# Kernel optimization log

Measured on AMD Instinct MI355X. Metric: run time of the kernel, lower is better.

The kernel has to match this reference:

```python
import jax, jax.numpy as jnp
import numpy as np


def conv1x1(x, W, b=None):
    # 1x1 conv == channel matmul: x (B,C,H,W), W (O,C)
    y = jnp.einsum('oc,bchw->bohw', W, x)
    if b is not None:
        y = y + b[None, :, None, None]
    return y


def setup_inputs() -> dict:
    key = jax.random.key(0)
    ks = jax.random.split(key, 20)
    B, C_l, C_h, H, W, d = 2, 64, 192, 64, 64, 128
    s = 0.02
    return {
        'll': jax.random.normal(ks[0], (B, C_l, H, W), jnp.float32),
        'hf': jax.random.normal(ks[1], (B, C_h, H, W), jnp.float32),
        'Wqh': jax.random.normal(ks[2], (d, C_h), jnp.float32) * s,
        'Wkh': jax.random.normal(ks[3], (d, C_h), jnp.float32) * s,
        'Wvh': jax.random.normal(ks[4], (d, C_h), jnp.float32) * s,
        'Wql': jax.random.normal(ks[5], (d, C_l), jnp.float32) * s,
        'Wkl': jax.random.normal(ks[6], (d, C_l), jnp.float32) * s,
        'Wvl': jax.random.normal(ks[7], (d, C_l), jnp.float32) * s,
        'Wph': jax.random.normal(ks[8], (C_h, d), jnp.float32) * s,
        'bph': jnp.zeros((C_h,), jnp.float32),
        'Wpl': jax.random.normal(ks[9], (C_l, d), jnp.float32) * s,
        'bpl': jnp.zeros((C_l,), jnp.float32),
        'Wah': jax.random.normal(ks[10], (C_h, C_h), jnp.float32) * s,
        'bah': jnp.zeros((C_h,), jnp.float32),
        'Wal': jax.random.normal(ks[11], (C_l, C_l), jnp.float32) * s,
        'bal': jnp.zeros((C_l,), jnp.float32),
        'alpha': jnp.ones((4,), jnp.float32),
    }


def reference(ll, hf, Wqh, Wkh, Wvh, Wql, Wkl, Wvl, Wph, bph, Wpl, bpl,
              Wah, bah, Wal, bal, alpha):
    B, C_l, H, W = ll.shape
    d = Wqh.shape[0]
    N = H * W
    scl = d ** (-0.5)

    Qh = conv1x1(hf, Wqh).reshape(B, d, N)
    Kh = conv1x1(hf, Wkh).reshape(B, d, N)
    Vh = conv1x1(hf, Wvh).reshape(B, d, N)
    Ql = conv1x1(ll, Wql).reshape(B, d, N)
    Kl = conv1x1(ll, Wkl).reshape(B, d, N)
    Vl = conv1x1(ll, Wvl).reshape(B, d, N)

    wdir = jax.nn.softmax(alpha)  # [row, col, diag, global]

    def sdpa(q, k, v):  # q,k,v: (B, L, d)
        a = jax.nn.softmax(jnp.einsum('bqd,bkd->bqk', q, k) * scl, axis=-1)
        return jnp.einsum('bqk,bkd->bqd', a, v)

    # ---- global: full N x N cross attention ----
    OL = sdpa(Qh.transpose(0, 2, 1), Kl.transpose(0, 2, 1), Vl.transpose(0, 2, 1)).transpose(0, 2, 1)
    OH = sdpa(Ql.transpose(0, 2, 1), Kh.transpose(0, 2, 1), Vh.transpose(0, 2, 1)).transpose(0, 2, 1)
    out_ll = conv1x1(OL.reshape(B, d, H, W), Wpl, bpl) * wdir[3]
    out_hf = conv1x1(OH.reshape(B, d, H, W), Wph, bph) * wdir[3]

    # ---- axial (row / col) attention ----
    def axial(q, k, v, row):
        perm = (0, 2, 3, 1) if row else (0, 3, 2, 1)  # (B,S,L,d)
        qr = q.reshape(B, d, H, W).transpose(perm)
        kr = k.reshape(B, d, H, W).transpose(perm)
        vr = v.reshape(B, d, H, W).transpose(perm)
        a = jax.nn.softmax(jnp.einsum('bsqd,bskd->bsqk', qr, kr) * scl, axis=-1)
        o = jnp.einsum('bsqk,bskd->bsqd', a, vr)
        inv = (0, 3, 1, 2) if row else (0, 3, 2, 1)
        return o.transpose(inv)  # (B,d,H,W)

    out_ll = out_ll + conv1x1(axial(Qh, Kl, Vl, True), Wpl, bpl) * wdir[0]
    out_hf = out_hf + conv1x1(axial(Ql, Kh, Vh, True), Wph, bph) * wdir[0]
    out_ll = out_ll + conv1x1(axial(Qh, Kl, Vl, False), Wpl, bpl) * wdir[1]
    out_hf = out_hf + conv1x1(axial(Ql, Kh, Vh, False), Wph, bph) * wdir[1]

    # ---- diag: faithful to original code (gather by diag index, attend, scatter back) ----
    i = jnp.arange(H)[:, None]
    j = jnp.arange(W)[None, :]
    flat_idx = (j - i + (H - 1)).reshape(-1)  # (N,), values in [0, H+W-2]

    def dsel(x):  # (B,d,N) -> (B,N,d) gathered along position axis
        return x[:, :, flat_idx].transpose(0, 2, 1)

    Ld = sdpa(dsel(Qh), dsel(Kl), dsel(Vl)).transpose(0, 2, 1)  # (B,d,N)
    Hd = sdpa(dsel(Ql), dsel(Kh), dsel(Vh)).transpose(0, 2, 1)
    blank_l = jnp.zeros((B, d, N), Ld.dtype).at[:, :, flat_idx].set(Ld)
    blank_h = jnp.zeros((B, d, N), Hd.dtype).at[:, :, flat_idx].set(Hd)
    out_ll = out_ll + conv1x1(blank_l.reshape(B, d, H, W), Wpl, bpl) * wdir[2]
    out_hf = out_hf + conv1x1(blank_h.reshape(B, d, H, W), Wph, bph) * wdir[2]

    ll_out = conv1x1(ll + out_ll, Wal, bal)
    hf_out = conv1x1(hf + out_hf, Wah, bah)
    return (ll_out, hf_out)
```

## Files before the change

kernel.cpp:

```cpp
#include <hip/hip_runtime.h>
#include <math.h>

#define N_  4096
#define D_  128
#define B_  2
#define CL_ 64
#define CH_ 192

typedef __attribute__((ext_vector_type(8))) short short8;
typedef __attribute__((ext_vector_type(4))) float f32x4;
typedef __attribute__((ext_vector_type(16))) float f32x16;

#if __has_builtin(__builtin_amdgcn_exp2f)
#define EXP2(x) __builtin_amdgcn_exp2f(x)
#else
#define EXP2(x) exp2f(x)
#endif

__device__ __forceinline__ short f2bf(float x) {
  union { float f; unsigned u; } v; v.f = x;
  unsigned r = v.u + 0x7FFFu + ((v.u >> 16) & 1u);
  return (short)(r >> 16);
}

typedef __attribute__((address_space(1))) const void gv_t;
typedef __attribute__((address_space(3))) void sv_t;
__device__ __forceinline__ void gl_lds16(const void* g, void* l) {
  __builtin_amdgcn_global_load_lds((gv_t*)g, (sv_t*)l, 16, 0, 0);
}

#define CVTPK(d, lo, hi) asm("v_cvt_pk_bf16_f32 %0, %1, %2" : "=v"(d) : "v"(lo), "v"(hi))
#define PLSWAP(a, b) asm("v_permlane32_swap_b32 %0, %1" : "+v"(a), "+v"(b))

__global__ __launch_bounds__(256)
void vt_kernel(const short* __restrict__ Vhb, const short* __restrict__ Vlb,
               short* __restrict__ Vht, short* __restrict__ Vlt) {
  __shared__ short rowbuf[4 * 4096];
  const int tid = threadIdx.x;
  const int lane = tid & 63, w = tid >> 6;
  const short* src = blockIdx.y ? Vlb : Vhb;
  short* dst = blockIdx.y ? Vlt : Vht;
  const int r0 = blockIdx.x * 4;
  #pragma unroll
  for (int i = 0; i < 8; ++i) {
    int idx = i * 256 + w * 64 + lane;
    int row = idx >> 9, g = idx & 511;
    gl_lds16(src + (size_t)(r0 + row) * N_ + g * 8,
             (char*)rowbuf + i * 4096 + w * 1024 + lane * 16);
  }
  __syncthreads();
  const int rw = r0 + w, d7 = rw & 7;
  const short* rb = rowbuf + w * 4096;
  const int w0 = (lane & 7) * 8, h0 = (lane >> 3) * 8;
  short8 rr[8];
  #pragma unroll
  for (int j = 0; j < 8; ++j)
    rr[j] = *(const short8*)(rb + (h0 + j) * 64 + (((w0 >> 3) ^ d7) * 8));
  #pragma unroll
  for (int i = 0; i < 8; ++i) {
    short8 o;
    #pragma unroll
    for (int j = 0; j < 8; ++j) o[j] = rr[j][i];
    *(short8*)(dst + (size_t)rw * N_ + (w0 + i) * 64 + (((h0 >> 3) ^ d7) * 8)) = o;
  }
}

struct QkvP {
  const float *W0h, *W1h, *W2h, *W0l, *W1l, *W2l;
  const float *Xh, *Xl;
  short *QbH, *KbH, *VbH, *QtH, *KtH;
  short *QbL, *KbL, *VbL, *QtL, *KtL;
  float qscale;
};

__global__ __launch_bounds__(256, 3)
void qkv_kernel(QkvP g) {
  __shared__ __align__(16) char BT[24576];
  __shared__ __align__(16) char AS[8192];
  __shared__ __align__(16) float Ls[64][67];
  const int tid = threadIdx.x;
  const int lane = tid & 63, w = tid >> 6, m = lane & 15, hi = lane >> 4;
  const int n0 = blockIdx.x * 64;
  const int sel = blockIdx.y >> 1, dhalf = blockIdx.y & 1, ot0 = dhalf * 64;
  const int b = blockIdx.z >> 1, s = blockIdx.z & 1;
  const int C = s ? CL_ : CH_;
  const float* Wm = s ? (sel == 0 ? g.W0l : sel == 1 ? g.W1l : g.W2l)
                      : (sel == 0 ? g.W0h : sel == 1 ? g.W1h : g.W2h);
  const float* Xs = (s ? g.Xl : g.Xh) + (size_t)b * C * N_;
  const int C2 = C * 2;

  for (int cc = 0; cc < C; cc += 64) {
    #pragma unroll
    for (int r = 0; r < 16; ++r) {
      int flat = r * 256 + tid;
      int c = flat >> 6, nn = flat & 63;
      Ls[c][nn] = Xs[(size_t)(cc + c) * N_ + n0 + nn];
    }
    __syncthreads();
    #pragma unroll
    for (int e = 0; e < 2; ++e) {
      int u = e * 256 + tid;
      int nn = u >> 3, gl = u & 7;
      short8 v;
      #pragma unroll
      for (int j = 0; j < 8; ++j) v[j] = f2bf(Ls[gl*8 + j][nn]);
      int pos = (gl ^ (nn & 7)) & 7;
      *(short8*)(BT + nn * C2 + cc * 2 + pos * 16) = v;
    }
    __syncthreads();
  }

  f32x4 acc[4];
  #pragma unroll
  for (int i = 0; i < 4; ++i) acc[i] = (f32x4){0.f, 0.f, 0.f, 0.f};

  for (int c0 = 0; c0 < C; c0 += 64) {
    __syncthreads();
    {
      int o = tid >> 2, cq = tid & 3;
      const float* wp = Wm + (size_t)(ot0 + o) * C + c0 + cq * 16;
      float4 fa = *(const float4*)(wp + 0);
      float4 fb = *(const float4*)(wp + 4);
      float4 fc = *(const float4*)(wp + 8);
      float4 fd = *(const float4*)(wp + 12);
      short8 v0 = { f2bf(fa.x), f2bf(fa.y), f2bf(fa.z), f2bf(fa.w),
                    f2bf(fb.x), f2bf(fb.y), f2bf(fb.z), f2bf(fb.w) };
      short8 v1 = { f2bf(fc.x), f2bf(fc.y), f2bf(fc.z), f2bf(fc.w),
                    f2bf(fd.x), f2bf(fd.y), f2bf(fd.z), f2bf(fd.w) };
      int g0 = cq * 2;
      *(short8*)(AS + o * 128 + (((g0) ^ (o & 7)) * 16)) = v0;
      *(short8*)(AS + o * 128 + (((g0 + 1) ^ (o & 7)) * 16)) = v1;
    }
    __syncthreads();
    const int orow = w * 16 + m;
    short8 a0 = *(const short8*)(AS + orow * 128 + (((hi) ^ (orow & 7)) * 16));
    short8 a1 = *(const short8*)(AS + orow * 128 + (((4 + hi) ^ (orow & 7)) * 16));
    #pragma unroll
    for (int nf = 0; nf < 4; ++nf) {
      int nrow = nf * 16 + m;
      const char* brow = BT + nrow * C2 + c0 * 2;
      short8 b0 = *(const short8*)(brow + (((hi) ^ (nrow & 7)) * 16));
      short8 b1 = *(const short8*)(brow + (((4 + hi) ^ (nrow & 7)) * 16));
      acc[nf] = __builtin_amdgcn_mfma_f32_16x16x32_bf16(a0, b0, acc[nf], 0, 0, 0);
      acc[nf] = __builtin_amdgcn_mfma_f32_16x16x32_bf16(a1, b1, acc[nf], 0, 0, 0);
    }
  }

  __syncthreads();
  #pragma unroll
  for (int nf = 0; nf < 4; ++nf)
    #pragma unroll
    for (int r = 0; r < 4; ++r)
      Ls[w * 16 + hi * 4 + r][nf * 16 + m] = acc[nf][r];
  __syncthreads();

  if (sel < 2) {
    float sc = (sel == 0) ? g.qscale : 1.f;
    short* QK = (sel == 0 ? (s ? g.QbL : g.QbH) : (s ? g.KbL : g.KbH)) + (size_t)b * N_ * D_;
    short* QKt = (sel == 0 ? (s ? g.QtL : g.QtH) : (s ? g.KtL : g.KtH)) + (size_t)b * N_ * D_;
    const int bx = blockIdx.x;
    #pragma unroll
    for (int e = 0; e < 2; ++e) {
      int u = tid + 256 * e;
      int nn = u >> 3, gl = u & 7;
      short8 v;
      #pragma unroll
      for (int j = 0; j < 8; ++j) v[j] = f2bf(Ls[gl*8 + j][nn] * sc);
      int posb = (dhalf * 8) | ((gl ^ (nn & 7)) & 7);
      *(short8*)(QK + (size_t)(n0 + nn) * D_ + posb * 8) = v;
      int post = (dhalf * 8) | ((gl ^ (bx & 7)) & 7);
      *(short8*)(QKt + (size_t)(nn * 64 + bx) * D_ + post * 8) = v;
    }
  } else {
    short* Vb = (s ? g.VbL : g.VbH) + (size_t)b * D_ * N_;
    #pragma unroll
    for (int e = 0; e < 2; ++e) {
      int u = tid + 256 * e;
      int o = u >> 3, gl = u & 7;
      int d = ot0 + o;
      short8 v;
      #pragma unroll
      for (int j = 0; j < 8; ++j) v[j] = f2bf(Ls[o][gl*8 + j]);
      *(short8*)(Vb + (size_t)d * N_ + n0 + ((gl ^ (d & 7)) * 8)) = v;
    }
  }
}

struct SmP {
  const short *Qhb, *Qlb, *Khb, *Klb, *Vhb, *Vlb;
  const short *Qht, *Qlt, *Kht, *Klt, *Vht, *Vlt;
  float *Mrl, *Mrh, *Mcl, *Mch, *Mdl, *Mdh;
  const float* alpha;
};

__global__ __launch_bounds__(256, 3)
void attn_sm(SmP p) {
  __shared__ __align__(16) char smem[49152];
  const int tid = threadIdx.x;
  const int lane = tid & 63, w = tid >> 6, m = lane & 15, hi = lane >> 4;

  const int bxg = blockIdx.x;
  int variant, y, bz, qx;
  if (bxg < 256)      { variant = 0; y = bxg & 63;        bz = bxg >> 6;        qx = 0; }
  else if (bxg < 512) { variant = 1; y = (bxg-256) & 63;  bz = (bxg-256) >> 6;  qx = 0; }
  else                { variant = 2; y = 0;               bz = (bxg-512) >> 1;  qx = (bxg-512) & 1; }
  const int b = bz >> 1, pair = bz & 1;
  const int widx = variant;
  const int cwflag = (variant == 2);
  const int qbase = (variant == 2) ? qx * 64 : y * 64;
  const int kcol0 = (variant == 2) ? 0 : y * 64;
  const int Lk = (variant == 2) ? 127 : 64;
  const int lqloc = (variant == 2) ? (qx ? 63 : 64) : 64;

  const short *Qs, *Ks, *Vs;
  if (variant == 1) {
    Qs = pair ? p.Qlt : p.Qht; Ks = pair ? p.Kht : p.Klt; Vs = pair ? p.Vht : p.Vlt;
  } else {
    Qs = pair ? p.Qlb : p.Qhb; Ks = pair ? p.Khb : p.Klb; Vs = pair ? p.Vhb : p.Vlb;
  }
  Qs += (size_t)b * N_ * D_; Ks += (size_t)b * N_ * D_; Vs += (size_t)b * D_ * N_;
  float* Mout;
  if (variant == 0)      Mout = (pair ? p.Mrh : p.Mrl) + (size_t)b * D_ * N_;
  else if (variant == 1) Mout = (pair ? p.Mch : p.Mcl) + (size_t)b * D_ * N_;
  else                   Mout = (pair ? p.Mdh : p.Mdl) + (size_t)b * D_ * 128;

  float a0 = p.alpha[0], a1 = p.alpha[1], a2 = p.alpha[2], a3 = p.alpha[3];
  float am = fmaxf(fmaxf(a0, a1), fmaxf(a2, a3));
  float e0 = __expf(a0-am), e1 = __expf(a1-am), e2 = __expf(a2-am), e3 = __expf(a3-am);
  float wsel = (widx == 0 ? e0 : widx == 1 ? e1 : e2) / (e0 + e1 + e2 + e3);

  auto stageK = [&](int kt) {
    #pragma unroll
    for (int i = 0; i < 4; ++i) {
      int chunk = w * 4 + i;
      gl_lds16(Ks + (size_t)(kcol0 + kt*64) * D_ + chunk * 512 + lane * 8,
               smem + 16384 + chunk * 1024);
    }
  };
  auto stageV = [&](int kt) {
    #pragma unroll
    for (int i = 0; i < 4; ++i) {
      int chunk = w * 4 + i;
      gl_lds16(Vs + (size_t)(chunk*8 + (lane>>3)) * N_ + kcol0 + kt*64 + (lane&7)*8,
               smem + 32768 + chunk * 1024);
    }
  };
  #pragma unroll
  for (int i = 0; i < 4; ++i) {
    int chunk = w * 4 + i;
    gl_lds16(Qs + (size_t)qbase * D_ + chunk * 512 + lane * 8, smem + chunk * 1024);
  }
  stageK(0); stageV(0);
  __syncthreads();

  const int qrow = w * 16 + m;
  short8 qf[4];
  #pragma unroll
  for (int cs = 0; cs < 4; ++cs)
    qf[cs] = *(const short8*)(smem + qrow * 256 + ((cs*64 + hi*16) ^ ((qrow & 7) << 4)));
  __syncthreads();

  f32x4 oacc[8];
  #pragma unroll
  for (int i = 0; i < 8; ++i) oacc[i] = (f32x4){0.f, 0.f, 0.f, 0.f};
  float m_run[4] = {-INFINITY, -INFINITY, -INFINITY, -INFINITY};
  float l_run[4] = {0.f, 0.f, 0.f, 0.f};
  char* const pstrip = smem + w * 2048;
  const int NT = (Lk + 63) >> 6;

  for (int kt = 0; kt < NT; ++kt) {
    const char* Kc = smem + 16384;
    const char* Vc = smem + 32768;
    f32x4 sacc[4];
    #pragma unroll
    for (int kf = 0; kf < 4; ++kf) sacc[kf] = (f32x4){0.f, 0.f, 0.f, 0.f};
    #pragma unroll
    for (int kf = 0; kf < 4; ++kf) {
      const int krow = kf * 16 + m;
      const char* kr = Kc + krow * 256;
      #pragma unroll
      for (int cs = 0; cs < 4; ++cs) {
        short8 kfr = *(const short8*)(kr + ((cs*64 + hi*16) ^ ((krow & 7) << 4)));
        sacc[kf] = __builtin_amdgcn_mfma_f32_16x16x32_bf16(qf[cs], kfr, sacc[kf], 0, 0, 0);
      }
    }
    float cw[4];
    #pragma unroll
    for (int kf = 0; kf < 4; ++kf) {
      if (cwflag) {
        int kg = kt * 64 + kf * 16 + m;
        int dd = kg - 63; dd = dd < 0 ? -dd : dd;
        cw[kf] = (kg < Lk) ? (float)(64 - dd) : 0.f;
      } else cw[kf] = 1.f;
    }
    #pragma unroll
    for (int r = 0; r < 4; ++r) {
      float mt = fmaxf(fmaxf(sacc[0][r], sacc[1][r]), fmaxf(sacc[2][r], sacc[3][r]));
      mt = fmaxf(mt, __shfl_xor(mt, 1));
      mt = fmaxf(mt, __shfl_xor(mt, 2));
      mt = fmaxf(mt, __shfl_xor(mt, 4));
      mt = fmaxf(mt, __shfl_xor(mt, 8));
      float mn = fmaxf(m_run[r], mt);
      float corr = EXP2(m_run[r] - mn);
      m_run[r] = mn;
      const int rl = hi * 4 + r;
      char* prow = pstrip + rl * 128;
      float psum = 0.f;
      #pragma unroll
      for (int kf = 0; kf < 4; ++kf) {
        float pv = cw[kf] * EXP2(sacc[kf][r] - mn);
        psum += pv;
        int kcol = (kf * 16 + m) * 2;
        *(short*)(prow + (kcol ^ ((rl & 7) << 4))) = f2bf(pv);
      }
      psum += __shfl_xor(psum, 1);
      psum += __shfl_xor(psum, 2);
      psum += __shfl_xor(psum, 4);
      psum += __shfl_xor(psum, 8);
      l_run[r] = l_run[r] * corr + psum;
      #pragma unroll
      for (int cf = 0; cf < 8; ++cf) oacc[cf][r] *= corr;
    }
    #pragma unroll
    for (int ks = 0; ks < 2; ++ks) {
      short8 pa = *(const short8*)(pstrip + m * 128 + ((ks*64 + hi*16) ^ ((m & 7) << 4)));
      #pragma unroll
      for (int cf = 0; cf < 8; ++cf) {
        const int crow = cf * 16 + m;
        short8 vf = *(const short8*)(Vc + crow * 128 + ((ks*64 + hi*16) ^ ((crow & 7) << 4)));
        oacc[cf] = __builtin_amdgcn_mfma_f32_16x16x32_bf16(pa, vf, oacc[cf], 0, 0, 0);
      }
    }
    __syncthreads();
    if (kt + 1 < NT) { stageK(kt + 1); stageV(kt + 1); __syncthreads(); }
  }

  float inv[4];
  #pragma unroll
  for (int r = 0; r < 4; ++r) inv[r] = wsel / l_run[r];
  float* Os = (float*)smem;
  #pragma unroll
  for (int cf = 0; cf < 8; ++cf)
    #pragma unroll
    for (int r = 0; r < 4; ++r)
      Os[(cf*16 + m) * 66 + w * 16 + hi * 4 + r] = oacc[cf][r] * inv[r];
  __syncthreads();
  for (int it = 0; it < 32; ++it) {
    int flat = it * 256 + tid;
    int c = flat >> 6, qq = flat & 63;
    if (qq < lqloc) {
      float v = Os[c * 66 + qq];
      if (variant == 0)      Mout[(size_t)c * N_ + qbase + qq] = v;
      else if (variant == 1) Mout[(size_t)c * N_ + qq * 64 + y] = v;
      else                   Mout[c * 128 + qbase + qq] = v;
    }
  }
}

#define GVQ 65536

struct GlobalAttnParams {
  const short *Qhb, *Qlb, *Khb, *Klb, *Vhb, *Vlb;
  const float *Mrl, *Mrh, *Mcl, *Mch, *Mdl, *Mdh;
  short *Mtbl, *Mtbh;
  const float* alpha;
};

__global__ __launch_bounds__(512, 1)
void attn_gl_kernel(GlobalAttnParams p) {
  __shared__ __align__(16) char smem[131072];
  const int tid = threadIdx.x;
  const int lane = tid & 63, w = tid >> 6;
  const int wid = w & 1, gsel = w >> 1;
  const int key = lane & 31, kh = lane >> 5;

  const int bx = blockIdx.x;
  const int xcd = bx & 7, sub = bx >> 3;
  const int pz = xcd >> 1;
  const int b = pz >> 1, pair = pz & 1;
  const int q0 = ((xcd & 1) * 32 + sub) * 64;

  const short* Qb = (pair ? p.Qlb : p.Qhb) + (size_t)b * N_ * D_;
  const short* Kb = (pair ? p.Khb : p.Klb) + (size_t)b * N_ * D_;
  const short* Vb = (pair ? p.Vhb : p.Vlb) + (size_t)b * D_ * N_;
  const float* Mr = (pair ? p.Mrh : p.Mrl) + (size_t)b * D_ * N_;
  const float* Mc = (pair ? p.Mch : p.Mcl) + (size_t)b * D_ * N_;
  const float* Md = (pair ? p.Mdh : p.Mdl) + (size_t)b * D_ * 128;
  short* Mtb = (pair ? p.Mtbh : p.Mtbl) + (size_t)b * N_ * D_;

  float a0 = p.alpha[0], a1 = p.alpha[1], a2 = p.alpha[2], a3 = p.alpha[3];
  float am = fmaxf(fmaxf(a0,a1), fmaxf(a2,a3));
  float e0 = __expf(a0-am), e1 = __expf(a1-am), e2 = __expf(a2-am), e3 = __expf(a3-am);
  const float wsel = e3 / (e0+e1+e2+e3);

  auto stageQuad = [&](int qd) {
    #pragma unroll
    for (int i = 0; i < 8; ++i) {
      int c = w*8 + i;
      if (c < 32) {
        int tk = c >> 3, ck = c & 7;
        gl_lds16(Kb + (size_t)((4*qd + tk)*32 + ck*4)*D_ + lane*8,
                 smem + (qd & 1)*32768 + tk*8192 + ck*1024);
      } else {
        int cc = c - 32;
        int d = cc*4 + (lane >> 4);
        int g = lane & 15, kb2 = g >> 3, gg = g & 7;
        gl_lds16(Vb + (size_t)d*N_ + qd*128 + kb2*64 + ((gg ^ (d & 7))*8),
                 smem + GVQ + (qd & 1)*32768 + cc*1024);
      }
    }
  };

  const int qq = wid*32 + key;
  const short* qrow_g = Qb + (size_t)(q0 + qq) * D_;
  short8 qf[8];
  #pragma unroll
  for (int fi = 0; fi < 8; ++fi)
    qf[fi] = *(const short8*)(qrow_g + (((fi*2 + kh) ^ (qq & 7)) << 3));

  stageQuad(0);

  f32x16 oacc[4];
  #pragma unroll
  for (int d = 0; d < 4; ++d)
    #pragma unroll
    for (int r = 0; r < 16; ++r) oacc[d][r] = 0.f;
  float m_run = -INFINITY, l_run = 0.f;

  const int NQ = N_ / 128;
  for (int j = 0; j < NQ; ++j) {
    __syncthreads();
    if (j + 1 < NQ) stageQuad(j + 1);

    const char* Kc = smem + (j & 1)*32768 + gsel*8192;
    const char* Vc = smem + GVQ + (j & 1)*32768;

    f32x16 sacc;
    #pragma unroll
    for (int r = 0; r < 16; ++r) sacc[r] = 0.f;
    __builtin_amdgcn_s_setprio(1);
    #pragma unroll
    for (int fi = 0; fi < 8; ++fi) {
      short8 kf = *(const short8*)(Kc + key*256 + (((fi*2 + kh) ^ (key & 7)) << 4));
      sacc = __builtin_amdgcn_mfma_f32_32x32x16_bf16(kf, qf[fi], sacc, 0, 0, 0);
    }
    __builtin_amdgcn_s_setprio(0);

    float mt = sacc[0];
    #pragma unroll
    for (int r = 1; r < 16; ++r) mt = fmaxf(mt, sacc[r]);
    { float aa = mt, bb = mt; PLSWAP(aa, bb); mt = fmaxf(aa, bb); }
    if (!__all(mt <= m_run + 8.f)) {
      float mn = fmaxf(m_run, mt);
      float corr = EXP2(m_run - mn);
      m_run = mn;
      l_run *= corr;
      #pragma unroll
      for (int d = 0; d < 4; ++d)
        #pragma unroll
        for (int r = 0; r < 16; ++r) oacc[d][r] *= corr;
    }
    float pv[16];
    float psum = 0.f;
    #pragma unroll
    for (int r = 0; r < 16; ++r) { pv[r] = EXP2(sacc[r] - m_run); psum += pv[r]; }
    { float sa = psum, sb = psum; PLSWAP(sa, sb); psum = sa + sb; }
    l_run += psum;

    union U8 { unsigned u[4]; short8 s; } pf0, pf1;
    {
      unsigned c0, c1, c2, c3;
      CVTPK(c0, pv[0], pv[1]);  CVTPK(c1, pv[2], pv[3]);
      CVTPK(c2, pv[4], pv[5]);  CVTPK(c3, pv[6], pv[7]);
      PLSWAP(c0, c2); PLSWAP(c1, c3);
      pf0.u[0] = c0; pf0.u[1] = c1; pf0.u[2] = c2; pf0.u[3] = c3;
      CVTPK(c0, pv[8],  pv[9]);  CVTPK(c1, pv[10], pv[11]);
      CVTPK(c2, pv[12], pv[13]); CVTPK(c3, pv[14], pv[15]);
      PLSWAP(c0, c2); PLSWAP(c1, c3);
      pf1.u[0] = c0; pf1.u[1] = c1; pf1.u[2] = c2; pf1.u[3] = c3;
    }

    __builtin_amdgcn_s_setprio(1);
    #pragma unroll
    for (int d = 0; d < 4; ++d) {
      #pragma unroll
      for (int ks = 0; ks < 2; ++ks) {
        int crow = d*32 + key;
        int gidx = gsel*4 + ks*2 + kh;
        int kb2 = gidx >> 3, gg = gidx & 7;
        short8 vf = *(const short8*)(Vc + crow*256 + kb2*128 + ((gg ^ (key & 7)) << 4));
        oacc[d] = __builtin_amdgcn_mfma_f32_32x32x16_bf16(vf, (ks ? pf1.s : pf0.s), oacc[d], 0, 0, 0);
      }
    }
    __builtin_amdgcn_s_setprio(0);
  }
  __syncthreads();

  float* MLbase = (float*)(smem + 98304);
  if (gsel > 0) {
    int idx = (gsel - 1)*2 + wid;
    float* ob = (float*)smem + idx*4096;
    #pragma unroll
    for (int d = 0; d < 4; ++d)
      #pragma unroll
      for (int r = 0; r < 16; ++r)
        ob[(d*16 + r)*64 + lane] = oacc[d][r];
    float* ml = MLbase + idx*128;
    ml[lane] = m_run;
    ml[64 + lane] = l_run;
  }
  __syncthreads();

  float inv = 0.f;
  if (gsel == 0) {
    float mp[3], lp[3];
    float mn = m_run;
    #pragma unroll
    for (int pi = 0; pi < 3; ++pi) {
      const float* ml = MLbase + (pi*2 + wid)*128;
      mp[pi] = ml[lane]; lp[pi] = ml[64 + lane];
      mn = fmaxf(mn, mp[pi]);
    }
    float cA = EXP2(m_run - mn);
    float lt = l_run * cA;
    #pragma unroll
    for (int d = 0; d < 4; ++d)
      #pragma unroll
      for (int r = 0; r < 16; ++r) oacc[d][r] *= cA;
    #pragma unroll
    for (int pi = 0; pi < 3; ++pi) {
      float cp = EXP2(mp[pi] - mn);
      lt += lp[pi] * cp;
      const float* ob = (const float*)smem + (pi*2 + wid)*4096;
      #pragma unroll
      for (int d = 0; d < 4; ++d)
        #pragma unroll
        for (int r = 0; r < 16; ++r)
          oacc[d][r] += ob[(d*16 + r)*64 + lane] * cp;
    }
    inv = wsel / lt;
  }
  __syncthreads();

  float* Os = (float*)smem;
  if (gsel == 0) {
    #pragma unroll
    for (int d = 0; d < 4; ++d)
      #pragma unroll
      for (int r = 0; r < 16; ++r) {
        int dr = d*32 + (r & 3) + 8*(r >> 2) + 4*kh;
        Os[dr*66 + qq] = oacc[d][r] * inv;
      }
  }
  __syncthreads();

  for (int it = 0; it < 16; ++it) {
    int flat = it*512 + tid;
    int c = flat >> 6, q2 = flat & 63;
    int pos = q0 + q2;
    float add = Mr[(size_t)c*N_ + pos] + Mc[(size_t)c*N_ + pos];
    if (pos < 127) add += Md[c*128 + pos];
    Os[c*66 + q2] += add;
  }
  __syncthreads();
  #pragma unroll
  for (int e = 0; e < 2; ++e) {
    int u = tid + 512*e;
    int nn = u >> 4, gb = u & 15;
    short8 v;
    #pragma unroll
    for (int jj = 0; jj < 8; ++jj) v[jj] = f2bf(Os[(gb*8 + jj)*66 + nn]);
    int pos = (gb & 8) | ((gb ^ (nn & 7)) & 7);
    *(short8*)(Mtb + (size_t)(q0 + nn)*D_ + pos*8) = v;
  }
}

struct Gemm2P {
  const float *WA; const short *BA; const float *resA, *biasA; float *outA; short *UtA; int KA, OA;
  const float *WB; const short *BB; const float *resB, *biasB; float *outB; short *UtB; int KB, OB;
  int ysplit, epmode;
};

__global__ __launch_bounds__(256, 4)
void gemm2_bf16(Gemm2P g) {
  __shared__ __align__(16) char AB[16384];
  __shared__ float Epi[64][67];
  const int tid = threadIdx.x;
  const int lane = tid & 63, w = tid >> 6, m = lane & 15, hi = lane >> 4;
  const int n0 = blockIdx.x * 64;
  const int b = blockIdx.z;
  const int yy = blockIdx.y;
  const bool isB = yy >= g.ysplit;
  const int ot0 = (isB ? (yy - g.ysplit) : yy) * 64;
  const float* Wm = isB ? g.WB : g.WA;
  const int K = isB ? g.KB : g.KA;
  const int O = isB ? g.OB : g.OA;
  const short* Bs = (isB ? g.BB : g.BA) + (size_t)b * N_ * K;

  f32x4 acc[4];
  #pragma unroll
  for (int i = 0; i < 4; ++i) acc[i] = (f32x4){0.f, 0.f, 0.f, 0.f};

  for (int c0 = 0; c0 < K; c0 += 64) {
    __syncthreads();
    {
      int o = tid >> 2, cq = tid & 3;
      const float* wp = Wm + (size_t)(ot0 + o) * K + c0 + cq * 16;
      float4 fa = *(const float4*)(wp + 0);
      float4 fb = *(const float4*)(wp + 4);
      float4 fc = *(const float4*)(wp + 8);
      float4 fd = *(const float4*)(wp + 12);
      short8 v0 = { f2bf(fa.x), f2bf(fa.y), f2bf(fa.z), f2bf(fa.w),
                    f2bf(fb.x), f2bf(fb.y), f2bf(fb.z), f2bf(fb.w) };
      short8 v1 = { f2bf(fc.x), f2bf(fc.y), f2bf(fc.z), f2bf(fc.w),
                    f2bf(fd.x), f2bf(fd.y), f2bf(fd.z), f2bf(fd.w) };
      int g0 = cq * 2;
      *(short8*)(AB + o * 128 + (((g0) ^ (o & 7)) * 16)) = v0;
      *(short8*)(AB + o * 128 + (((g0 + 1) ^ (o & 7)) * 16)) = v1;
    }
    #pragma unroll
    for (int e = 0; e < 2; ++e) {
      int cid = e * 256 + w * 64 + lane;
      int nn = cid >> 3, gs = cid & 7;
      gl_lds16(Bs + (size_t)(n0 + nn) * K + c0 + gs * 8,
               AB + 8192 + e * 4096 + w * 1024 + lane * 16);
    }
    __syncthreads();
    const int orow = w * 16 + m;
    short8 a0 = *(const short8*)(AB + orow * 128 + (((hi) ^ (orow & 7)) * 16));
    short8 a1 = *(const short8*)(AB + orow * 128 + (((4 + hi) ^ (orow & 7)) * 16));
    #pragma unroll
    for (int nf = 0; nf < 4; ++nf) {
      int nrow = nf * 16 + m;
      short8 b0 = *(const short8*)(AB + 8192 + nrow * 128 + (((hi) ^ (nrow & 7)) * 16));
      short8 b1 = *(const short8*)(AB + 8192 + nrow * 128 + (((4 + hi) ^ (nrow & 7)) * 16));
      acc[nf] = __builtin_amdgcn_mfma_f32_16x16x32_bf16(a0, b0, acc[nf], 0, 0, 0);
      acc[nf] = __builtin_amdgcn_mfma_f32_16x16x32_bf16(a1, b1, acc[nf], 0, 0, 0);
    }
  }

  #pragma unroll
  for (int nf = 0; nf < 4; ++nf)
    #pragma unroll
    for (int r = 0; r < 4; ++r)
      Epi[w * 16 + hi * 4 + r][nf * 16 + m] = acc[nf][r];
  __syncthreads();

  if (g.epmode == 1) {
    const float* res = (isB ? g.resB : g.resA) + (size_t)b * O * N_;
    const float* bias = isB ? g.biasB : g.biasA;
    short* Ut = (isB ? g.UtB : g.UtA) + (size_t)b * N_ * O;
    #pragma unroll
    for (int e = 0; e < 2; ++e) {
      int nn = tid & 63;
      int gl = (tid >> 6) + e * 4;
      int ob = ot0 + gl * 8;
      short8 v;
      #pragma unroll
      for (int j = 0; j < 8; ++j)
        v[j] = f2bf(Epi[gl*8 + j][nn] + res[(size_t)(ob + j) * N_ + n0 + nn] + bias[ob + j]);
      int gout = (ot0 >> 3) + gl;
      int pos = (gout & ~7) | ((gout ^ (nn & 7)) & 7);
      *(short8*)(Ut + (size_t)(n0 + nn) * O + pos * 8) = v;
    }
  } else {
    const float* bias = isB ? g.biasB : g.biasA;
    float* outF = isB ? g.outB : g.outA;
    int o = tid >> 2, nq = tid & 3;
    float bv = bias[ot0 + o];
    float* dst = outF + (size_t)b * O * N_ + (size_t)(ot0 + o) * N_ + n0 + nq * 16;
    #pragma unroll
    for (int q4 = 0; q4 < 4; ++q4) {
      float4 vv = { Epi[o][nq*16 + q4*4 + 0] + bv, Epi[o][nq*16 + q4*4 + 1] + bv,
                    Epi[o][nq*16 + q4*4 + 2] + bv, Epi[o][nq*16 + q4*4 + 3] + bv };
      *(float4*)(dst + q4 * 4) = vv;
    }
  }
}

extern "C" void kernel_launch(void* const* d_in, const int* in_sizes, int n_in,
                              void* d_out, int out_size, void* d_ws, size_t ws_size,
                              hipStream_t stream) {
  (void)in_sizes; (void)n_in; (void)out_size; (void)ws_size;
  const float* ll  = (const float*)d_in[0];
  const float* hf  = (const float*)d_in[1];
  const float* Wqh = (const float*)d_in[2];
  const float* Wkh = (const float*)d_in[3];
  const float* Wvh = (const float*)d_in[4];
  const float* Wql = (const float*)d_in[5];
  const float* Wkl = (const float*)d_in[6];
  const float* Wvl = (const float*)d_in[7];
  const float* Wph = (const float*)d_in[8];
  const float* bph = (const float*)d_in[9];
  const float* Wpl = (const float*)d_in[10];
  const float* bpl = (const float*)d_in[11];
  const float* Wah = (const float*)d_in[12];
  const float* bah = (const float*)d_in[13];
  const float* Wal = (const float*)d_in[14];
  const float* bal = (const float*)d_in[15];
  const float* alpha = (const float*)d_in[16];

  float* ws = (float*)d_ws;
  const size_t BDN = (size_t)B_ * D_ * N_;
  float* Mrl = ws;
  float* Mrh = Mrl + BDN;
  float* Mcl = Mrh + BDN;
  float* Mch = Mcl + BDN;
  float* Mdl = Mch + BDN;
  float* Mdh = Mdl + (size_t)B_ * D_ * 128;
  short* sp = (short*)(Mdh + (size_t)B_ * D_ * 128);
  short* Qhb = sp;           sp += BDN;
  short* Qlb = sp;           sp += BDN;
  short* Khb = sp;           sp += BDN;
  short* Klb = sp;           sp += BDN;
  short* Vhb = sp;           sp += BDN;
  short* Vlb = sp;           sp += BDN;
  short* Qht = sp;           sp += BDN;
  short* Qlt = sp;           sp += BDN;
  short* Kht = sp;           sp += BDN;
  short* Klt = sp;           sp += BDN;
  short* Vht = sp;           sp += BDN;
  short* Vlt = sp;           sp += BDN;
  short* Mtbl = Qht;
  short* Mtbh = Qlt;
  short* Utl  = Kht;
  short* Uth  = Klt;

  dim3 blk(256, 1, 1);
  const float qscale = (float)(0.08838834764831845 * 1.4426950408889634);
  float* out = (float*)d_out;

  QkvP qp{Wqh, Wkh, Wvh, Wql, Wkl, Wvl, hf, ll,
          Qhb, Khb, Vhb, Qht, Kht, Qlb, Klb, Vlb, Qlt, Klt, qscale};
  qkv_kernel<<<dim3(N_/64, 6, 2*B_), blk, 0, stream>>>(qp);

  vt_kernel<<<dim3(64, 2), blk, 0, stream>>>(Vhb, Vlb, Vht, Vlt);

  SmP smp{Qhb, Qlb, Khb, Klb, Vhb, Vlb, Qht, Qlt, Kht, Klt, Vht, Vlt,
          Mrl, Mrh, Mcl, Mch, Mdl, Mdh, alpha};
  attn_sm<<<dim3(520, 1, 1), blk, 0, stream>>>(smp);

  GlobalAttnParams gp{Qhb, Qlb, Khb, Klb, Vhb, Vlb,
                      Mrl, Mrh, Mcl, Mch, Mdl, Mdh, Mtbl, Mtbh, alpha};
  attn_gl_kernel<<<dim3(256, 1, 1), dim3(512,1,1), 0, stream>>>(gp);

  Gemm2P wp{Wpl, Mtbl, ll, bpl, nullptr, Utl, D_, CL_,
            Wph, Mtbh, hf, bph, nullptr, Uth, D_, CH_, 1, 1};
  gemm2_bf16<<<dim3(N_/64, 4, B_), blk, 0, stream>>>(wp);

  Gemm2P wa{Wal, Utl, nullptr, bal, out, nullptr, CL_, CL_,
            Wah, Uth, nullptr, bah, out + (size_t)B_*CL_*N_, nullptr, CH_, CH_, 1, 2};
  gemm2_bf16<<<dim3(N_/64, 4, B_), blk, 0, stream>>>(wa);
}
```

Baseline: 119.5 us.

## Double waves per block in global attention with single-buffered 256-key tiles

The global attention kernel now launches 1024 threads (16 waves) per block instead of 512, so eight wave groups split each 256-key tile in place of four splitting each 128-key tile. The double-buffered K/V staging is replaced by a single buffer that is loaded and synchronised at the top of each iteration, with a barrier at the end. The split-K partial outputs are combined by a two-level reduction through shared memory, and the shared-memory layout moves to accommodate it. This aims to hide latency through more waves per CU, but loses the prefetch overlap and adds barriers and reduction work.

```diff
diff --git a/kernel.cpp b/kernel.cpp
--- a/kernel.cpp
+++ b/kernel.cpp
@@ -357,7 +357,9 @@
   }
 }
 
-#define GVQ 65536
+#define GVO  65536
+#define SLOT 16896
+#define OSOFF 101376
 
 struct GlobalAttnParams {
   const short *Qhb, *Qlb, *Khb, *Klb, *Vhb, *Vlb;
@@ -366,9 +368,9 @@
   const float* alpha;
 };
 
-__global__ __launch_bounds__(512, 1)
+__global__ __launch_bounds__(1024, 4)
 void attn_gl_kernel(GlobalAttnParams p) {
-  __shared__ __align__(16) char smem[131072];
+  __shared__ __align__(16) char smem[139264];
   const int tid = threadIdx.x;
   const int lane = tid & 63, w = tid >> 6;
   const int wid = w & 1, gsel = w >> 1;
@@ -393,20 +395,20 @@
   float e0 = __expf(a0-am), e1 = __expf(a1-am), e2 = __expf(a2-am), e3 = __expf(a3-am);
   const float wsel = e3 / (e0+e1+e2+e3);
 
-  auto stageQuad = [&](int qd) {
+  auto stageOct = [&](int qd) {
     #pragma unroll
     for (int i = 0; i < 8; ++i) {
       int c = w*8 + i;
-      if (c < 32) {
+      if (c < 64) {
         int tk = c >> 3, ck = c & 7;
-        gl_lds16(Kb + (size_t)((4*qd + tk)*32 + ck*4)*D_ + lane*8,
-                 smem + (qd & 1)*32768 + tk*8192 + ck*1024);
+        gl_lds16(Kb + (size_t)((8*qd + tk)*32 + ck*4)*D_ + lane*8,
+                 smem + tk*8192 + ck*1024);
       } else {
-        int cc = c - 32;
-        int d = cc*4 + (lane >> 4);
-        int g = lane & 15, kb2 = g >> 3, gg = g & 7;
-        gl_lds16(Vb + (size_t)d*N_ + qd*128 + kb2*64 + ((gg ^ (d & 7))*8),
-                 smem + GVQ + (qd & 1)*32768 + cc*1024);
+        int cc = c - 64;
+        int d = cc*2 + (lane >> 5);
+        int g = lane & 31, kb2 = g >> 3, gg = g & 7;
+        gl_lds16(Vb + (size_t)d*N_ + qd*256 + kb2*64 + ((gg ^ (d & 7))*8),
+                 smem + GVO + cc*1024);
       }
     }
   };
@@ -418,8 +420,6 @@
   for (int fi = 0; fi < 8; ++fi)
     qf[fi] = *(const short8*)(qrow_g + (((fi*2 + kh) ^ (qq & 7)) << 3));
 
-  stageQuad(0);
-
   f32x16 oacc[4];
   #pragma unroll
   for (int d = 0; d < 4; ++d)
@@ -427,13 +427,13 @@
     for (int r = 0; r < 16; ++r) oacc[d][r] = 0.f;
   float m_run = -INFINITY, l_run = 0.f;
 
-  const int NQ = N_ / 128;
+  const int NQ = N_ / 256;
   for (int j = 0; j < NQ; ++j) {
-    __syncthreads();
-    if (j + 1 < NQ) stageQuad(j + 1);
-
-    const char* Kc = smem + (j & 1)*32768 + gsel*8192;
-    const char* Vc = smem + GVQ + (j & 1)*32768;
+    stageOct(j);
+    __syncthreads();
+
+    const char* Kc = smem + gsel*8192;
+    const char* Vc = smem + GVO;
 
     f32x16 sacc;
     #pragma unroll
@@ -488,36 +488,63 @@
         int crow = d*32 + key;
         int gidx = gsel*4 + ks*2 + kh;
         int kb2 = gidx >> 3, gg = gidx & 7;
-        short8 vf = *(const short8*)(Vc + crow*256 + kb2*128 + ((gg ^ (key & 7)) << 4));
+        short8 vf = *(const short8*)(Vc + crow*512 + kb2*128 + ((gg ^ (crow & 7)) << 4));
         oacc[d] = __builtin_amdgcn_mfma_f32_32x32x16_bf16(vf, (ks ? pf1.s : pf0.s), oacc[d], 0, 0, 0);
       }
     }
     __builtin_amdgcn_s_setprio(0);
-  }
-  __syncthreads();
-
-  float* MLbase = (float*)(smem + 98304);
-  if (gsel > 0) {
-    int idx = (gsel - 1)*2 + wid;
-    float* ob = (float*)smem + idx*4096;
+    __syncthreads();
+  }
+
+  if (gsel >= 4) {
+    int idx = (gsel - 4)*2 + wid;
+    float* ob = (float*)(smem + idx*SLOT);
     #pragma unroll
     for (int d = 0; d < 4; ++d)
       #pragma unroll
       for (int r = 0; r < 16; ++r)
         ob[(d*16 + r)*64 + lane] = oacc[d][r];
-    float* ml = MLbase + idx*128;
+    float* ml = (float*)(smem + idx*SLOT + 16384);
     ml[lane] = m_run;
     ml[64 + lane] = l_run;
   }
   __syncthreads();
-
-  float inv = 0.f;
+  if (gsel < 4) {
+    int idx = gsel*2 + wid;
+    const float* ob = (const float*)(smem + idx*SLOT);
+    const float* ml = (const float*)(smem + idx*SLOT + 16384);
+    float mB = ml[lane], lB = ml[64 + lane];
+    float mn = fmaxf(m_run, mB);
+    float cA = EXP2(m_run - mn), cB = EXP2(mB - mn);
+    #pragma unroll
+    for (int d = 0; d < 4; ++d)
+      #pragma unroll
+      for (int r = 0; r < 16; ++r)
+        oacc[d][r] = oacc[d][r]*cA + ob[(d*16 + r)*64 + lane]*cB;
+    l_run = l_run*cA + lB*cB;
+    m_run = mn;
+  }
+  __syncthreads();
+  if (gsel >= 1 && gsel < 4) {
+    int idx = (gsel - 1)*2 + wid;
+    float* ob = (float*)(smem + idx*SLOT);
+    #pragma unroll
+    for (int d = 0; d < 4; ++d)
+      #pragma unroll
+      for (int r = 0; r < 16; ++r)
+        ob[(d*16 + r)*64 + lane] = oacc[d][r];
+    float* ml = (float*)(smem + idx*SLOT + 16384);
+    ml[lane] = m_run;
+    ml[64 + lane] = l_run;
+  }
+  __syncthreads();
+  float* Os = (float*)(smem + OSOFF);
   if (gsel == 0) {
     float mp[3], lp[3];
     float mn = m_run;
     #pragma unroll
     for (int pi = 0; pi < 3; ++pi) {
-      const float* ml = MLbase + (pi*2 + wid)*128;
+      const float* ml = (const float*)(smem + (pi*2 + wid)*SLOT + 16384);
       mp[pi] = ml[lane]; lp[pi] = ml[64 + lane];
       mn = fmaxf(mn, mp[pi]);
     }
@@ -531,19 +558,14 @@
     for (int pi = 0; pi < 3; ++pi) {
       float cp = EXP2(mp[pi] - mn);
       lt += lp[pi] * cp;
-      const float* ob = (const float*)smem + (pi*2 + wid)*4096;
+      const float* ob = (const float*)(smem + (pi*2 + wid)*SLOT);
       #pragma unroll
       for (int d = 0; d < 4; ++d)
         #pragma unroll
         for (int r = 0; r < 16; ++r)
           oacc[d][r] += ob[(d*16 + r)*64 + lane] * cp;
     }
-    inv = wsel / lt;
-  }
-  __syncthreads();
-
-  float* Os = (float*)smem;
-  if (gsel == 0) {
+    float inv = wsel / lt;
     #pragma unroll
     for (int d = 0; d < 4; ++d)
       #pragma unroll
@@ -554,8 +576,8 @@
   }
   __syncthreads();
 
-  for (int it = 0; it < 16; ++it) {
-    int flat = it*512 + tid;
+  for (int it = 0; it < 8; ++it) {
+    int flat = it*1024 + tid;
     int c = flat >> 6, q2 = flat & 63;
     int pos = q0 + q2;
     float add = Mr[(size_t)c*N_ + pos] + Mc[(size_t)c*N_ + pos];
@@ -563,9 +585,8 @@
     Os[c*66 + q2] += add;
   }
   __syncthreads();
-  #pragma unroll
-  for (int e = 0; e < 2; ++e) {
-    int u = tid + 512*e;
+  {
+    int u = tid;
     int nn = u >> 4, gb = u & 15;
     short8 v;
     #pragma unroll
@@ -742,7 +763,7 @@
 
   GlobalAttnParams gp{Qhb, Qlb, Khb, Klb, Vhb, Vlb,
                       Mrl, Mrh, Mcl, Mch, Mdl, Mdh, Mtbl, Mtbh, alpha};
-  attn_gl_kernel<<<dim3(256, 1, 1), dim3(512,1,1), 0, stream>>>(gp);
+  attn_gl_kernel<<<dim3(256, 1, 1), dim3(1024,1,1), 0, stream>>>(gp);
 
   Gemm2P wp{Wpl, Mtbl, ll, bpl, nullptr, Utl, D_, CL_,
             Wph, Mtbh, hf, bph, nullptr, Uth, D_, CH_, 1, 1};
```

Result: slower. 178.6 us (+49.4%).
